# Performance work log

Measured on AMD Instinct MI355X. Metric: run time of the kernel, lower is better.

Reference implementation:

```python
import jax, jax.numpy as jnp
import numpy as np

B, L, H, NH, NB = 8, 200, 128, 4, 2
HD = H // NH
ITEM_NUM, TIME_SPAN = 50000, 256
PAD = -2.0**32 + 1.0


def setup_inputs() -> dict:
    key = jax.random.key(0)
    ks = jax.random.split(key, 32)
    def g(i, shape, s=0.02):
        return jax.random.normal(ks[i], shape, jnp.float32) * s
    item_emb = g(0, (ITEM_NUM + 1, H)).at[0].set(0.0)  # padding_idx=0
    return dict(
        user_ids=jax.random.randint(ks[1], (B,), 0, 1000),
        log_seqs=jax.random.randint(ks[2], (B, L), 0, ITEM_NUM),
        time_matrices=jax.random.randint(ks[3], (B, L, L), 0, TIME_SPAN + 1),
        pos_seqs=jax.random.randint(ks[4], (B, L), 0, ITEM_NUM + 1),
        neg_seqs=jax.random.randint(ks[5], (B, L), 0, ITEM_NUM + 1),
        item_emb=item_emb,
        pos_K_emb=g(6, (L, H)), pos_V_emb=g(7, (L, H)),
        time_K_emb=g(8, (TIME_SPAN + 1, H)), time_V_emb=g(9, (TIME_SPAN + 1, H)),
        attn_ln_g=jnp.ones((NB, H)), attn_ln_b=jnp.zeros((NB, H)),
        Wq=g(10, (NB, H, H)), bq=jnp.zeros((NB, H)),
        Wk=g(11, (NB, H, H)), bk=jnp.zeros((NB, H)),
        Wv=g(12, (NB, H, H)), bv=jnp.zeros((NB, H)),
        fwd_ln_g=jnp.ones((NB, H)), fwd_ln_b=jnp.zeros((NB, H)),
        W1=g(13, (NB, H, H)), b1=jnp.zeros((NB, H)),
        W2=g(14, (NB, H, H)), b2=jnp.zeros((NB, H)),
        last_ln_g=jnp.ones((H,)), last_ln_b=jnp.zeros((H,)),
    )


def _ln(x, g, b, eps=1e-8):
    m = x.mean(-1, keepdims=True)
    v = jnp.var(x, axis=-1, keepdims=True)
    return (x - m) / jnp.sqrt(v + eps) * g + b


def _heads(x):
    # [..., H] -> [NH, ..., HD]; matches torch.cat(torch.split(x, HD, -1), 0)
    y = x.reshape(x.shape[:-1] + (NH, HD))
    return jnp.moveaxis(y, -2, 0)


def reference(user_ids, log_seqs, time_matrices, pos_seqs, neg_seqs, item_emb,
              pos_K_emb, pos_V_emb, time_K_emb, time_V_emb,
              attn_ln_g, attn_ln_b, Wq, bq, Wk, bk, Wv, bv,
              fwd_ln_g, fwd_ln_b, W1, b1, W2, b2, last_ln_g, last_ln_b):
    # user_ids is unused in the original forward as well.
    tmask = log_seqs == 0                                  # [B,L] True = pad
    keep = (~tmask)[..., None].astype(jnp.float32)
    seqs = item_emb[log_seqs] * np.float32(np.sqrt(H))
    seqs = seqs * keep
    pKh = _heads(pos_K_emb)                                # [NH,L,HD]
    pVh = _heads(pos_V_emb)
    tKh = _heads(time_K_emb[time_matrices])                # [NH,B,L,L,HD]
    tVh = _heads(time_V_emb[time_matrices])
    causal = ~jnp.tril(jnp.ones((L, L), bool))             # True above diag -> masked
    bad = tmask[:, :, None] | causal[None]                 # [B,L,L]
    scale = np.float32(np.sqrt(HD))
    for i in range(NB):
        Qin = _ln(seqs, attn_ln_g[i], attn_ln_b[i])
        Qh = _heads(Qin @ Wq[i].T + bq[i])                 # [NH,B,L,HD]
        Kh = _heads(seqs @ Wk[i].T + bk[i])
        Vh = _heads(seqs @ Wv[i].T + bv[i])
        attn = (jnp.einsum('nbqd,nbkd->nbqk', Qh, Kh)
                + jnp.einsum('nbqd,nkd->nbqk', Qh, pKh)
                + jnp.einsum('nbqkd,nbqd->nbqk', tKh, Qh)) / scale
        attn = jnp.where(bad[None], PAD, attn)
        attn = jax.nn.softmax(attn, axis=-1)
        out = (jnp.einsum('nbqk,nbkd->nbqd', attn, Vh)
               + jnp.einsum('nbqk,nkd->nbqd', attn, pVh)
               + jnp.einsum('nbqk,nbqkd->nbqd', attn, tVh))
        out = jnp.moveaxis(out, 0, -2).reshape(seqs.shape)  # merge heads -> [B,L,H]
        seqs = Qin + out                                    # residual uses LN'd Q (as in source)
        seqs = _ln(seqs, fwd_ln_g[i], fwd_ln_b[i])
        ff = jax.nn.relu(seqs @ W1[i].T + b1[i]) @ W2[i].T + b2[i] + seqs
        seqs = ff * keep
    log_feats = _ln(seqs, last_ln_g, last_ln_b)
    pos_logits = (log_feats * item_emb[pos_seqs]).sum(-1)   # [B,L]
    neg_logits = (log_feats * item_emb[neg_seqs]).sum(-1)
    return pos_logits, neg_logits
```

## Files before the change

kernel.cpp:

```cpp
#include <hip/hip_runtime.h>
#include <hip/hip_bf16.h>

#define BB 8
#define LL 200
#define HH 128
#define NHEAD 4
#define HDIM 32
#define NBLK 2
#define BL (BB * LL)
#define NT 257
#define QT 8
#define NQT 25
#define SSP 208
#define KTP 66

static constexpr float SQRT_H    = 11.313708498984761f;
static constexpr float INV_SCALE = 0.17677669529663687f;
static constexpr float PADV      = -4294967295.0f;

__global__ void k_lnqkv(const float* __restrict__ seqs_in,
                        const int* __restrict__ log_seqs,
                        const float* __restrict__ item_emb,
                        const float* __restrict__ g, const float* __restrict__ bia,
                        const float* __restrict__ Wq, const float* __restrict__ bq,
                        const float* __restrict__ Wk, const float* __restrict__ bk,
                        const float* __restrict__ Wv, const float* __restrict__ bv,
                        const float* __restrict__ posK, const float* __restrict__ posV,
                        float* __restrict__ Qin, float* __restrict__ Q,
                        float* __restrict__ K, float* __restrict__ V) {
    int row0 = blockIdx.x * 4;
    int tid = threadIdx.x;
    int wv = tid >> 6, ln = tid & 63;
    __shared__ float xT[HH][8];
    __shared__ float Wst[3 * HH * 33];

    for (int rr = 0; rr < 2; rr++) {
        int r = 2 * wv + rr;
        int row = row0 + r;
        float v0, v1;
        if (seqs_in) {
            v0 = seqs_in[(size_t)row * HH + ln];
            v1 = seqs_in[(size_t)row * HH + ln + 64];
        } else {
            int idx = log_seqs[row];
            if (idx == 0) { v0 = 0.f; v1 = 0.f; }
            else {
                v0 = item_emb[(size_t)idx * HH + ln] * SQRT_H;
                v1 = item_emb[(size_t)idx * HH + ln + 64] * SQRT_H;
            }
        }
        float s = v0 + v1, s2 = v0 * v0 + v1 * v1;
        for (int off = 32; off; off >>= 1) {
            s  += __shfl_xor(s, off);
            s2 += __shfl_xor(s2, off);
        }
        float mean = s * (1.f / HH);
        float var  = s2 * (1.f / HH) - mean * mean;
        float inv  = 1.f / sqrtf(var + 1e-8f);
        float q0v = (v0 - mean) * inv * g[ln]      + bia[ln];
        float q1v = (v1 - mean) * inv * g[ln + 64] + bia[ln + 64];
        xT[ln][r] = q0v;      xT[ln + 64][r] = q1v;
        xT[ln][4 + r] = v0;   xT[ln + 64][4 + r] = v1;
        Qin[(size_t)row * HH + ln]      = q0v;
        Qin[(size_t)row * HH + ln + 64] = q1v;
    }
    __syncthreads();

    int j = tid;
    float aq[4] = {0,0,0,0}, ak[4] = {0,0,0,0}, av[4] = {0,0,0,0};
    for (int c = 0; c < 4; c++) {
        #pragma unroll
        for (int m = 0; m < 3; m++) {
            const float* Wm = (m == 0) ? Wq : (m == 1) ? Wk : Wv;
            #pragma unroll
            for (int p = 0; p < 8; p++) {
                int idx = tid + p * 128;
                int jj = idx >> 3, k4 = idx & 7;
                float4 w = *(const float4*)(Wm + (size_t)jj * HH + c * 32 + k4 * 4);
                float* dst = &Wst[m * HH * 33 + jj * 33 + k4 * 4];
                dst[0] = w.x; dst[1] = w.y; dst[2] = w.z; dst[3] = w.w;
            }
        }
        __syncthreads();
        #pragma unroll 4
        for (int kk = 0; kk < 32; kk++) {
            int k = c * 32 + kk;
            float4 xq4 = *(const float4*)&xT[k][0];
            float4 xs4 = *(const float4*)&xT[k][4];
            float wq = Wst[0 * HH * 33 + j * 33 + kk];
            float wk = Wst[1 * HH * 33 + j * 33 + kk];
            float wvv = Wst[2 * HH * 33 + j * 33 + kk];
            aq[0] += xq4.x * wq; aq[1] += xq4.y * wq; aq[2] += xq4.z * wq; aq[3] += xq4.w * wq;
            ak[0] += xs4.x * wk; ak[1] += xs4.y * wk; ak[2] += xs4.z * wk; ak[3] += xs4.w * wk;
            av[0] += xs4.x * wvv; av[1] += xs4.y * wvv; av[2] += xs4.z * wvv; av[3] += xs4.w * wvv;
        }
        __syncthreads();
    }
    float bqv = bq[j], bkv = bk[j], bvv = bv[j];
    #pragma unroll
    for (int r = 0; r < 4; r++) {
        int row = row0 + r;
        int l = row % LL;
        Q[(size_t)row * HH + j] = (aq[r] + bqv) * INV_SCALE;
        K[(size_t)row * HH + j] = ak[r] + bkv + posK[l * HH + j];
        V[(size_t)row * HH + j] = av[r] + bvv + posV[l * HH + j];
    }
}

__global__ void k_attn(const float* __restrict__ Q, const float* __restrict__ K,
                       const float* __restrict__ V,
                       const float* __restrict__ timeK, const float* __restrict__ timeV,
                       const int* __restrict__ tm,
                       float* __restrict__ att) {
    int bn = blockIdx.x & 31;
    int b = bn >> 2, n = bn & 3;
    int qt = (NQT - 1) - (blockIdx.x >> 5);
    int q0 = qt * QT;
    int kmax = q0 + QT - 1;
    int tid = threadIdx.x;
    int wv = tid >> 6, ln = tid & 63;

    __shared__ float Qs[QT * HDIM];
    __shared__ float KstT[HDIM * KTP];
    __shared__ float DTW[QT * NT];
    __shared__ float Ssc[QT * SSP];
    __shared__ int   tmst[QT * LL];
    __shared__ float Ost[QT * HDIM];

    Ost[tid] = 0.f;
    if (tid < 64) {
        int qi = tid >> 3, d4 = tid & 7;
        *(float4*)(Qs + qi * HDIM + d4 * 4) =
            *(const float4*)(Q + ((size_t)(b * LL + q0 + qi)) * HH + n * HDIM + d4 * 4);
    }
    #pragma unroll
    for (int qi = 0; qi < QT; qi++)
        if (tid < LL)
            tmst[qi * LL + tid] = tm[((size_t)(b * LL + q0 + qi)) * LL + tid];
    __syncthreads();

    int k2 = tid & 31, qi_c = tid >> 5;

    for (int c = 0; c < 5; c++) {
        #pragma unroll
        for (int p = 0; p < 2; p++) {
            int idx = tid + p * 256;
            int r = idx >> 3, d4 = idx & 7;
            int tau = c * 64 + r;
            float4 w = make_float4(0.f, 0.f, 0.f, 0.f);
            if (tau < NT) w = *(const float4*)(timeK + (size_t)tau * HH + n * HDIM + d4 * 4);
            KstT[(d4 * 4 + 0) * KTP + r] = w.x;
            KstT[(d4 * 4 + 1) * KTP + r] = w.y;
            KstT[(d4 * 4 + 2) * KTP + r] = w.z;
            KstT[(d4 * 4 + 3) * KTP + r] = w.w;
        }
        __syncthreads();
        float a0 = 0.f, a1 = 0.f;
        #pragma unroll 4
        for (int d = 0; d < HDIM; d++) {
            float qv = Qs[qi_c * HDIM + d];
            float2 kv = *(const float2*)&KstT[d * KTP + k2 * 2];
            a0 += qv * kv.x; a1 += qv * kv.y;
        }
        int tau0 = c * 64 + k2 * 2;
        if (tau0 < NT)     DTW[qi_c * NT + tau0]     = a0;
        if (tau0 + 1 < NT) DTW[qi_c * NT + tau0 + 1] = a1;
        __syncthreads();
    }

    int nch = (kmax >> 6) + 1;
    for (int c = 0; c < nch; c++) {
        #pragma unroll
        for (int p = 0; p < 2; p++) {
            int idx = tid + p * 256;
            int r = idx >> 3, d4 = idx & 7;
            int k = c * 64 + r;
            float4 w = make_float4(0.f, 0.f, 0.f, 0.f);
            if (k < LL) w = *(const float4*)(K + ((size_t)(b * LL + k)) * HH + n * HDIM + d4 * 4);
            KstT[(d4 * 4 + 0) * KTP + r] = w.x;
            KstT[(d4 * 4 + 1) * KTP + r] = w.y;
            KstT[(d4 * 4 + 2) * KTP + r] = w.z;
            KstT[(d4 * 4 + 3) * KTP + r] = w.w;
        }
        __syncthreads();
        float a0 = 0.f, a1 = 0.f;
        #pragma unroll 4
        for (int d = 0; d < HDIM; d++) {
            float qv = Qs[qi_c * HDIM + d];
            float2 kv = *(const float2*)&KstT[d * KTP + k2 * 2];
            a0 += qv * kv.x; a1 += qv * kv.y;
        }
        int q = q0 + qi_c;
        int k0 = c * 64 + k2 * 2;
        if (k0 <= kmax)
            Ssc[qi_c * SSP + k0] = (k0 <= q) ? (a0 + DTW[qi_c * NT + tmst[qi_c * LL + k0]]) : PADV;
        if (k0 + 1 <= kmax)
            Ssc[qi_c * SSP + k0 + 1] = (k0 + 1 <= q) ? (a1 + DTW[qi_c * NT + tmst[qi_c * LL + k0 + 1]]) : PADV;
        __syncthreads();
    }

    for (int idx = tid; idx < QT * NT; idx += 256) DTW[idx] = 0.f;
    __syncthreads();

    for (int rr = 0; rr < 2; rr++) {
        int qi = wv + rr * 4;
        int q = q0 + qi;
        float sv[4];
        float m = PADV;
        #pragma unroll
        for (int jj = 0; jj < 4; jj++) {
            int k = ln + 64 * jj;
            sv[jj] = (k <= q) ? Ssc[qi * SSP + k] : PADV;
            m = fmaxf(m, sv[jj]);
        }
        for (int off = 32; off; off >>= 1) m = fmaxf(m, __shfl_xor(m, off));
        float sum = 0.f;
        #pragma unroll
        for (int jj = 0; jj < 4; jj++) {
            int k = ln + 64 * jj;
            sv[jj] = (k <= q) ? __expf(sv[jj] - m) : 0.f;
            sum += sv[jj];
        }
        for (int off = 32; off; off >>= 1) sum += __shfl_xor(sum, off);
        float inv = 1.f / sum;
        #pragma unroll
        for (int jj = 0; jj < 4; jj++) {
            int k = ln + 64 * jj;
            float p = sv[jj] * inv;
            if (k < SSP) Ssc[qi * SSP + k] = (k <= q) ? p : 0.f;
            if (k <= q) atomicAdd(&DTW[qi * NT + tmst[qi * LL + k]], p);
        }
    }
    __syncthreads();

    int d = tid & 31, kg = tid >> 5;
    float acc[QT] = {0,0,0,0,0,0,0,0};
    const float* vb = V + ((size_t)(b * LL)) * HH + n * HDIM + d;
    for (int k = kg; k <= kmax; k += 8) {
        float v = vb[(size_t)k * HH];
        #pragma unroll
        for (int qi = 0; qi < QT; qi++) acc[qi] += Ssc[qi * SSP + k] * v;
    }
    const float* tvb = timeV + n * HDIM + d;
    for (int t = kg; t < NT; t += 8) {
        float v = tvb[(size_t)t * HH];
        #pragma unroll
        for (int qi = 0; qi < QT; qi++) acc[qi] += DTW[qi * NT + t] * v;
    }
    #pragma unroll
    for (int qi = 0; qi < QT; qi++) atomicAdd(&Ost[qi * HDIM + d], acc[qi]);
    __syncthreads();
    {
        int qi = tid >> 5;
        att[((size_t)(b * LL + q0 + qi)) * HH + n * HDIM + d] = Ost[qi * HDIM + d];
    }
}

__global__ void k_lnffn(const float* __restrict__ Qin, const float* __restrict__ att,
                        const float* __restrict__ g, const float* __restrict__ bia,
                        const float* __restrict__ W1, const float* __restrict__ b1,
                        const float* __restrict__ W2, const float* __restrict__ b2,
                        const int* __restrict__ log_seqs, float* __restrict__ out) {
    int row0 = blockIdx.x * 4;
    int tid = threadIdx.x;
    int wv = tid >> 6, ln = tid & 63;
    __shared__ float xT[HH][8];
    __shared__ float Wst[HH * 33];

    for (int rr = 0; rr < 2; rr++) {
        int r = 2 * wv + rr;
        int row = row0 + r;
        float v0 = Qin[(size_t)row * HH + ln]      + att[(size_t)row * HH + ln];
        float v1 = Qin[(size_t)row * HH + ln + 64] + att[(size_t)row * HH + ln + 64];
        float s = v0 + v1, s2 = v0 * v0 + v1 * v1;
        for (int off = 32; off; off >>= 1) {
            s  += __shfl_xor(s, off);
            s2 += __shfl_xor(s2, off);
        }
        float mean = s * (1.f / HH);
        float var  = s2 * (1.f / HH) - mean * mean;
        float inv  = 1.f / sqrtf(var + 1e-8f);
        xT[ln][r]      = (v0 - mean) * inv * g[ln]      + bia[ln];
        xT[ln + 64][r] = (v1 - mean) * inv * g[ln + 64] + bia[ln + 64];
    }
    __syncthreads();

    int j = tid;
    float a[4] = {0,0,0,0};
    for (int c = 0; c < 4; c++) {
        #pragma unroll
        for (int p = 0; p < 8; p++) {
            int idx = tid + p * 128;
            int jj = idx >> 3, k4 = idx & 7;
            float4 w = *(const float4*)(W1 + (size_t)jj * HH + c * 32 + k4 * 4);
            float* dst = &Wst[jj * 33 + k4 * 4];
            dst[0] = w.x; dst[1] = w.y; dst[2] = w.z; dst[3] = w.w;
        }
        __syncthreads();
        #pragma unroll 4
        for (int kk = 0; kk < 32; kk++) {
            int k = c * 32 + kk;
            float4 x4 = *(const float4*)&xT[k][0];
            float w = Wst[j * 33 + kk];
            a[0] += x4.x * w; a[1] += x4.y * w; a[2] += x4.z * w; a[3] += x4.w * w;
        }
        __syncthreads();
    }
    float b1v = b1[j];
    #pragma unroll
    for (int r = 0; r < 4; r++) {
        float t = a[r] + b1v;
        xT[j][4 + r] = t > 0.f ? t : 0.f;
    }
    __syncthreads();

    float c2[4] = {0,0,0,0};
    for (int c = 0; c < 4; c++) {
        #pragma unroll
        for (int p = 0; p < 8; p++) {
            int idx = tid + p * 128;
            int jj = idx >> 3, k4 = idx & 7;
            float4 w = *(const float4*)(W2 + (size_t)jj * HH + c * 32 + k4 * 4);
            float* dst = &Wst[jj * 33 + k4 * 4];
            dst[0] = w.x; dst[1] = w.y; dst[2] = w.z; dst[3] = w.w;
        }
        __syncthreads();
        #pragma unroll 4
        for (int kk = 0; kk < 32; kk++) {
            int k = c * 32 + kk;
            float4 x4 = *(const float4*)&xT[k][4];
            float w = Wst[j * 33 + kk];
            c2[0] += x4.x * w; c2[1] += x4.y * w; c2[2] += x4.z * w; c2[3] += x4.w * w;
        }
        __syncthreads();
    }
    float b2v = b2[j];
    float4 y4 = *(const float4*)&xT[j][0];
    float yv[4] = {y4.x, y4.y, y4.z, y4.w};
    #pragma unroll
    for (int r = 0; r < 4; r++) {
        int row = row0 + r;
        float t = c2[r] + b2v + yv[r];
        out[(size_t)row * HH + j] = (log_seqs[row] == 0) ? 0.f : t;
    }
}

__global__ void k_lnlogits(const float* __restrict__ seqs,
                           const float* __restrict__ g, const float* __restrict__ bia,
                           const float* __restrict__ item_emb,
                           const int* __restrict__ pos, const int* __restrict__ neg,
                           float* __restrict__ out) {
    int row = blockIdx.x;
    int h = threadIdx.x;
    float v = seqs[(size_t)row * HH + h];
    float s = v, s2 = v * v;
    for (int off = 32; off; off >>= 1) {
        s  += __shfl_xor(s, off);
        s2 += __shfl_xor(s2, off);
    }
    __shared__ float r1[2], r2[2];
    if ((h & 63) == 0) { r1[h >> 6] = s; r2[h >> 6] = s2; }
    __syncthreads();
    float mean = (r1[0] + r1[1]) * (1.f / HH);
    float var  = (r2[0] + r2[1]) * (1.f / HH) - mean * mean;
    float inv = 1.f / sqrtf(var + 1e-8f);
    float f = (v - mean) * inv * g[h] + bia[h];

    int ip = pos[row], in_ = neg[row];
    float vp = f * item_emb[(size_t)ip * HH + h];
    float vn = f * item_emb[(size_t)in_ * HH + h];
    for (int off = 32; off; off >>= 1) {
        vp += __shfl_xor(vp, off);
        vn += __shfl_xor(vn, off);
    }
    __shared__ float rp[2], rn[2];
    if ((h & 63) == 0) { rp[h >> 6] = vp; rn[h >> 6] = vn; }
    __syncthreads();
    if (h == 0) {
        out[row]      = rp[0] + rp[1];
        out[BL + row] = rn[0] + rn[1];
    }
}

extern "C" void kernel_launch(void* const* d_in, const int* in_sizes, int n_in,
                              void* d_out, int out_size, void* d_ws, size_t ws_size,
                              hipStream_t stream) {
    const int* log_seqs   = (const int*)d_in[1];
    const int* tm         = (const int*)d_in[2];
    const int* pos_seqs   = (const int*)d_in[3];
    const int* neg_seqs   = (const int*)d_in[4];
    const float* item_emb = (const float*)d_in[5];
    const float* posK     = (const float*)d_in[6];
    const float* posV     = (const float*)d_in[7];
    const float* timeK    = (const float*)d_in[8];
    const float* timeV    = (const float*)d_in[9];
    const float* attn_g   = (const float*)d_in[10];
    const float* attn_b   = (const float*)d_in[11];
    const float* Wq       = (const float*)d_in[12];
    const float* bq       = (const float*)d_in[13];
    const float* Wk       = (const float*)d_in[14];
    const float* bk       = (const float*)d_in[15];
    const float* Wv       = (const float*)d_in[16];
    const float* bv       = (const float*)d_in[17];
    const float* fwd_g    = (const float*)d_in[18];
    const float* fwd_b    = (const float*)d_in[19];
    const float* W1       = (const float*)d_in[20];
    const float* b1       = (const float*)d_in[21];
    const float* W2       = (const float*)d_in[22];
    const float* b2       = (const float*)d_in[23];
    const float* last_g   = (const float*)d_in[24];
    const float* last_b   = (const float*)d_in[25];

    float* seqs = (float*)d_ws;
    float* Qin  = seqs + (size_t)BL * HH;
    float* Qb   = Qin  + (size_t)BL * HH;
    float* Kb   = Qb   + (size_t)BL * HH;
    float* Vb   = Kb   + (size_t)BL * HH;
    float* att  = Vb   + (size_t)BL * HH;

    for (int i = 0; i < NBLK; i++) {
        k_lnqkv<<<BL / 4, 128, 0, stream>>>(i == 0 ? nullptr : seqs, log_seqs, item_emb,
                                            attn_g + i * HH, attn_b + i * HH,
                                            Wq + (size_t)i * HH * HH, bq + i * HH,
                                            Wk + (size_t)i * HH * HH, bk + i * HH,
                                            Wv + (size_t)i * HH * HH, bv + i * HH,
                                            posK, posV, Qin, Qb, Kb, Vb);
        k_attn<<<NQT * 32, 256, 0, stream>>>(Qb, Kb, Vb, timeK, timeV, tm, att);
        k_lnffn<<<BL / 4, 128, 0, stream>>>(Qin, att, fwd_g + i * HH, fwd_b + i * HH,
                                            W1 + (size_t)i * HH * HH, b1 + i * HH,
                                            W2 + (size_t)i * HH * HH, b2 + i * HH,
                                            log_seqs, seqs);
    }
    k_lnlogits<<<BL, HH, 0, stream>>>(seqs, last_g, last_b, item_emb,
                                      pos_seqs, neg_seqs, (float*)d_out);
}
```

Baseline: 269.9 us.

## Retile QKV and FFN projections as register-blocked GEMMs with larger row tiles

Replaces the 4-row-per-block QKV and fused FFN kernels with tiled GEMM kernels: QKV uses 32-row by 64-column tiles split across the three matrices, and the FFN is split into two kernels (ff1 with LN+W1+ReLU, ff2 with W2 plus residual recomputed from Qin+att). Each thread computes a small register tile from shared memory, and the full 128-wide K dimension is loaded at once. The aim is to cut how often weights are reloaded per row and to raise arithmetic intensity. In exchange it adds an extra launch, an h1 intermediate buffer round trip, and LayerNorm recomputed redundantly across column tiles.

```diff
diff --git a/kernel.cpp b/kernel.cpp
--- a/kernel.cpp
+++ b/kernel.cpp
@@ -13,97 +13,153 @@
 #define NQT 25
 #define SSP 208
 #define KTP 66
+#define ASP 36
+#define BSP 66
+#define FASP 20
+#define RSP 132
 
 static constexpr float SQRT_H    = 11.313708498984761f;
 static constexpr float INV_SCALE = 0.17677669529663687f;
 static constexpr float PADV      = -4294967295.0f;
 
-__global__ void k_lnqkv(const float* __restrict__ seqs_in,
-                        const int* __restrict__ log_seqs,
-                        const float* __restrict__ item_emb,
-                        const float* __restrict__ g, const float* __restrict__ bia,
-                        const float* __restrict__ Wq, const float* __restrict__ bq,
-                        const float* __restrict__ Wk, const float* __restrict__ bk,
-                        const float* __restrict__ Wv, const float* __restrict__ bv,
-                        const float* __restrict__ posK, const float* __restrict__ posV,
-                        float* __restrict__ Qin, float* __restrict__ Q,
-                        float* __restrict__ K, float* __restrict__ V) {
-    int row0 = blockIdx.x * 4;
+__global__ void k_qkv_gemm(const float* __restrict__ seqs_in,
+                           const int* __restrict__ log_seqs,
+                           const float* __restrict__ item_emb,
+                           const float* __restrict__ g, const float* __restrict__ bia,
+                           const float* __restrict__ Wq, const float* __restrict__ bq,
+                           const float* __restrict__ Wk, const float* __restrict__ bk,
+                           const float* __restrict__ Wv, const float* __restrict__ bv,
+                           const float* __restrict__ posK, const float* __restrict__ posV,
+                           float* __restrict__ Qin, float* __restrict__ Q,
+                           float* __restrict__ K, float* __restrict__ V) {
+    int mt = blockIdx.x / 6, nt = blockIdx.x % 6;
+    int matsel = nt >> 1;
+    int jb = (nt & 1) * 64;
+    int row0 = mt * 32;
     int tid = threadIdx.x;
-    int wv = tid >> 6, ln = tid & 63;
-    __shared__ float xT[HH][8];
-    __shared__ float Wst[3 * HH * 33];
-
-    for (int rr = 0; rr < 2; rr++) {
-        int r = 2 * wv + rr;
+    __shared__ float As[128 * ASP];
+    __shared__ float Bs[128 * BSP];
+
+    {
+        int r = tid >> 3, seg = tid & 7;
         int row = row0 + r;
-        float v0, v1;
+        float4 vv[4];
         if (seqs_in) {
-            v0 = seqs_in[(size_t)row * HH + ln];
-            v1 = seqs_in[(size_t)row * HH + ln + 64];
+            #pragma unroll
+            for (int i = 0; i < 4; i++)
+                vv[i] = *(const float4*)(seqs_in + (size_t)row * HH + seg * 16 + i * 4);
         } else {
             int idx = log_seqs[row];
-            if (idx == 0) { v0 = 0.f; v1 = 0.f; }
-            else {
-                v0 = item_emb[(size_t)idx * HH + ln] * SQRT_H;
-                v1 = item_emb[(size_t)idx * HH + ln + 64] * SQRT_H;
+            if (idx == 0) {
+                #pragma unroll
+                for (int i = 0; i < 4; i++) vv[i] = make_float4(0.f, 0.f, 0.f, 0.f);
+            } else {
+                #pragma unroll
+                for (int i = 0; i < 4; i++) {
+                    float4 e = *(const float4*)(item_emb + (size_t)idx * HH + seg * 16 + i * 4);
+                    vv[i] = make_float4(e.x * SQRT_H, e.y * SQRT_H, e.z * SQRT_H, e.w * SQRT_H);
+                }
             }
         }
-        float s = v0 + v1, s2 = v0 * v0 + v1 * v1;
-        for (int off = 32; off; off >>= 1) {
-            s  += __shfl_xor(s, off);
-            s2 += __shfl_xor(s2, off);
-        }
-        float mean = s * (1.f / HH);
-        float var  = s2 * (1.f / HH) - mean * mean;
-        float inv  = 1.f / sqrtf(var + 1e-8f);
-        float q0v = (v0 - mean) * inv * g[ln]      + bia[ln];
-        float q1v = (v1 - mean) * inv * g[ln + 64] + bia[ln + 64];
-        xT[ln][r] = q0v;      xT[ln + 64][r] = q1v;
-        xT[ln][4 + r] = v0;   xT[ln + 64][4 + r] = v1;
-        Qin[(size_t)row * HH + ln]      = q0v;
-        Qin[(size_t)row * HH + ln + 64] = q1v;
-    }
-    __syncthreads();
-
-    int j = tid;
-    float aq[4] = {0,0,0,0}, ak[4] = {0,0,0,0}, av[4] = {0,0,0,0};
-    for (int c = 0; c < 4; c++) {
-        #pragma unroll
-        for (int m = 0; m < 3; m++) {
-            const float* Wm = (m == 0) ? Wq : (m == 1) ? Wk : Wv;
+        if (matsel == 0) {
+            float s = 0.f, s2 = 0.f;
             #pragma unroll
-            for (int p = 0; p < 8; p++) {
-                int idx = tid + p * 128;
-                int jj = idx >> 3, k4 = idx & 7;
-                float4 w = *(const float4*)(Wm + (size_t)jj * HH + c * 32 + k4 * 4);
-                float* dst = &Wst[m * HH * 33 + jj * 33 + k4 * 4];
-                dst[0] = w.x; dst[1] = w.y; dst[2] = w.z; dst[3] = w.w;
+            for (int i = 0; i < 4; i++) {
+                s  += vv[i].x + vv[i].y + vv[i].z + vv[i].w;
+                s2 += vv[i].x * vv[i].x + vv[i].y * vv[i].y + vv[i].z * vv[i].z + vv[i].w * vv[i].w;
             }
-        }
-        __syncthreads();
-        #pragma unroll 4
-        for (int kk = 0; kk < 32; kk++) {
-            int k = c * 32 + kk;
-            float4 xq4 = *(const float4*)&xT[k][0];
-            float4 xs4 = *(const float4*)&xT[k][4];
-            float wq = Wst[0 * HH * 33 + j * 33 + kk];
-            float wk = Wst[1 * HH * 33 + j * 33 + kk];
-            float wvv = Wst[2 * HH * 33 + j * 33 + kk];
-            aq[0] += xq4.x * wq; aq[1] += xq4.y * wq; aq[2] += xq4.z * wq; aq[3] += xq4.w * wq;
-            ak[0] += xs4.x * wk; ak[1] += xs4.y * wk; ak[2] += xs4.z * wk; ak[3] += xs4.w * wk;
-            av[0] += xs4.x * wvv; av[1] += xs4.y * wvv; av[2] += xs4.z * wvv; av[3] += xs4.w * wvv;
-        }
-        __syncthreads();
-    }
-    float bqv = bq[j], bkv = bk[j], bvv = bv[j];
-    #pragma unroll
-    for (int r = 0; r < 4; r++) {
-        int row = row0 + r;
-        int l = row % LL;
-        Q[(size_t)row * HH + j] = (aq[r] + bqv) * INV_SCALE;
-        K[(size_t)row * HH + j] = ak[r] + bkv + posK[l * HH + j];
-        V[(size_t)row * HH + j] = av[r] + bvv + posV[l * HH + j];
+            #pragma unroll
+            for (int off = 1; off < 8; off <<= 1) {
+                s  += __shfl_xor(s, off);
+                s2 += __shfl_xor(s2, off);
+            }
+            float mean = s * (1.f / HH);
+            float var  = s2 * (1.f / HH) - mean * mean;
+            float inv  = 1.f / sqrtf(var + 1e-8f);
+            #pragma unroll
+            for (int i = 0; i < 4; i++) {
+                int k = seg * 16 + i * 4;
+                float4 g4 = *(const float4*)(g + k);
+                float4 b4 = *(const float4*)(bia + k);
+                float4 y;
+                y.x = (vv[i].x - mean) * inv * g4.x + b4.x;
+                y.y = (vv[i].y - mean) * inv * g4.y + b4.y;
+                y.z = (vv[i].z - mean) * inv * g4.z + b4.z;
+                y.w = (vv[i].w - mean) * inv * g4.w + b4.w;
+                As[(k + 0) * ASP + r] = y.x;
+                As[(k + 1) * ASP + r] = y.y;
+                As[(k + 2) * ASP + r] = y.z;
+                As[(k + 3) * ASP + r] = y.w;
+                if (nt == 0) *(float4*)(Qin + (size_t)row * HH + k) = y;
+            }
+        } else {
+            #pragma unroll
+            for (int i = 0; i < 4; i++) {
+                int k = seg * 16 + i * 4;
+                As[(k + 0) * ASP + r] = vv[i].x;
+                As[(k + 1) * ASP + r] = vv[i].y;
+                As[(k + 2) * ASP + r] = vv[i].z;
+                As[(k + 3) * ASP + r] = vv[i].w;
+            }
+        }
+    }
+    {
+        const float* W = (matsel == 0) ? Wq : (matsel == 1) ? Wk : Wv;
+        int k4 = tid & 31, jj0 = tid >> 5;
+        #pragma unroll
+        for (int p = 0; p < 8; p++) {
+            int jj = jj0 + p * 8;
+            float4 w = *(const float4*)(W + (size_t)(jb + jj) * HH + k4 * 4);
+            Bs[(k4 * 4 + 0) * BSP + jj] = w.x;
+            Bs[(k4 * 4 + 1) * BSP + jj] = w.y;
+            Bs[(k4 * 4 + 2) * BSP + jj] = w.z;
+            Bs[(k4 * 4 + 3) * BSP + jj] = w.w;
+        }
+    }
+    __syncthreads();
+
+    int my = tid >> 5, jx = tid & 31;
+    float a00=0,a01=0,a10=0,a11=0,a20=0,a21=0,a30=0,a31=0;
+    #pragma unroll 4
+    for (int k = 0; k < HH; k++) {
+        float4 a = *(const float4*)&As[k * ASP + my * 4];
+        float2 b = *(const float2*)&Bs[k * BSP + jx * 2];
+        a00 += a.x * b.x; a01 += a.x * b.y;
+        a10 += a.y * b.x; a11 += a.y * b.y;
+        a20 += a.z * b.x; a21 += a.z * b.y;
+        a30 += a.w * b.x; a31 += a.w * b.y;
+    }
+    float accs[4][2] = {{a00,a01},{a10,a11},{a20,a21},{a30,a31}};
+    int col = jb + jx * 2;
+    if (matsel == 0) {
+        float2 bb = *(const float2*)(bq + col);
+        #pragma unroll
+        for (int r = 0; r < 4; r++) {
+            int row = row0 + my * 4 + r;
+            float2 o = make_float2((accs[r][0] + bb.x) * INV_SCALE,
+                                   (accs[r][1] + bb.y) * INV_SCALE);
+            *(float2*)(Q + (size_t)row * HH + col) = o;
+        }
+    } else if (matsel == 1) {
+        float2 bb = *(const float2*)(bk + col);
+        #pragma unroll
+        for (int r = 0; r < 4; r++) {
+            int row = row0 + my * 4 + r;
+            int l = row % LL;
+            float2 pk = *(const float2*)(posK + (size_t)l * HH + col);
+            float2 o = make_float2(accs[r][0] + bb.x + pk.x, accs[r][1] + bb.y + pk.y);
+            *(float2*)(K + (size_t)row * HH + col) = o;
+        }
+    } else {
+        float2 bb = *(const float2*)(bv + col);
+        #pragma unroll
+        for (int r = 0; r < 4; r++) {
+            int row = row0 + my * 4 + r;
+            int l = row % LL;
+            float2 pv = *(const float2*)(posV + (size_t)l * HH + col);
+            float2 o = make_float2(accs[r][0] + bb.x + pv.x, accs[r][1] + bb.y + pv.y);
+            *(float2*)(V + (size_t)row * HH + col) = o;
+        }
     }
 }
 
@@ -256,92 +312,173 @@
     }
 }
 
-__global__ void k_lnffn(const float* __restrict__ Qin, const float* __restrict__ att,
-                        const float* __restrict__ g, const float* __restrict__ bia,
-                        const float* __restrict__ W1, const float* __restrict__ b1,
-                        const float* __restrict__ W2, const float* __restrict__ b2,
-                        const int* __restrict__ log_seqs, float* __restrict__ out) {
-    int row0 = blockIdx.x * 4;
+__global__ void k_ff1(const float* __restrict__ Qin, const float* __restrict__ att,
+                      const float* __restrict__ g, const float* __restrict__ bia,
+                      const float* __restrict__ W1, const float* __restrict__ b1,
+                      float* __restrict__ h1) {
+    int mt = blockIdx.x >> 1, nt = blockIdx.x & 1;
+    int jb = nt * 64;
+    int row0 = mt * 16;
     int tid = threadIdx.x;
-    int wv = tid >> 6, ln = tid & 63;
-    __shared__ float xT[HH][8];
-    __shared__ float Wst[HH * 33];
-
-    for (int rr = 0; rr < 2; rr++) {
-        int r = 2 * wv + rr;
+    __shared__ float As[128 * FASP];
+    __shared__ float Bs[128 * BSP];
+
+    {
+        int r = tid >> 4, seg = tid & 15;
         int row = row0 + r;
-        float v0 = Qin[(size_t)row * HH + ln]      + att[(size_t)row * HH + ln];
-        float v1 = Qin[(size_t)row * HH + ln + 64] + att[(size_t)row * HH + ln + 64];
-        float s = v0 + v1, s2 = v0 * v0 + v1 * v1;
-        for (int off = 32; off; off >>= 1) {
+        float4 vv[2];
+        #pragma unroll
+        for (int i = 0; i < 2; i++) {
+            int k = seg * 8 + i * 4;
+            float4 q4 = *(const float4*)(Qin + (size_t)row * HH + k);
+            float4 a4 = *(const float4*)(att + (size_t)row * HH + k);
+            vv[i] = make_float4(q4.x + a4.x, q4.y + a4.y, q4.z + a4.z, q4.w + a4.w);
+        }
+        float s = 0.f, s2 = 0.f;
+        #pragma unroll
+        for (int i = 0; i < 2; i++) {
+            s  += vv[i].x + vv[i].y + vv[i].z + vv[i].w;
+            s2 += vv[i].x * vv[i].x + vv[i].y * vv[i].y + vv[i].z * vv[i].z + vv[i].w * vv[i].w;
+        }
+        #pragma unroll
+        for (int off = 1; off < 16; off <<= 1) {
             s  += __shfl_xor(s, off);
             s2 += __shfl_xor(s2, off);
         }
         float mean = s * (1.f / HH);
         float var  = s2 * (1.f / HH) - mean * mean;
         float inv  = 1.f / sqrtf(var + 1e-8f);
-        xT[ln][r]      = (v0 - mean) * inv * g[ln]      + bia[ln];
-        xT[ln + 64][r] = (v1 - mean) * inv * g[ln + 64] + bia[ln + 64];
-    }
-    __syncthreads();
-
-    int j = tid;
-    float a[4] = {0,0,0,0};
-    for (int c = 0; c < 4; c++) {
+        #pragma unroll
+        for (int i = 0; i < 2; i++) {
+            int k = seg * 8 + i * 4;
+            float4 g4 = *(const float4*)(g + k);
+            float4 b4 = *(const float4*)(bia + k);
+            As[(k + 0) * FASP + r] = (vv[i].x - mean) * inv * g4.x + b4.x;
+            As[(k + 1) * FASP + r] = (vv[i].y - mean) * inv * g4.y + b4.y;
+            As[(k + 2) * FASP + r] = (vv[i].z - mean) * inv * g4.z + b4.z;
+            As[(k + 3) * FASP + r] = (vv[i].w - mean) * inv * g4.w + b4.w;
+        }
+    }
+    {
+        int k4 = tid & 31, jj0 = tid >> 5;
         #pragma unroll
         for (int p = 0; p < 8; p++) {
-            int idx = tid + p * 128;
-            int jj = idx >> 3, k4 = idx & 7;
-            float4 w = *(const float4*)(W1 + (size_t)jj * HH + c * 32 + k4 * 4);
-            float* dst = &Wst[jj * 33 + k4 * 4];
-            dst[0] = w.x; dst[1] = w.y; dst[2] = w.z; dst[3] = w.w;
-        }
-        __syncthreads();
-        #pragma unroll 4
-        for (int kk = 0; kk < 32; kk++) {
-            int k = c * 32 + kk;
-            float4 x4 = *(const float4*)&xT[k][0];
-            float w = Wst[j * 33 + kk];
-            a[0] += x4.x * w; a[1] += x4.y * w; a[2] += x4.z * w; a[3] += x4.w * w;
-        }
-        __syncthreads();
-    }
-    float b1v = b1[j];
+            int jj = jj0 + p * 8;
+            float4 w = *(const float4*)(W1 + (size_t)(jb + jj) * HH + k4 * 4);
+            Bs[(k4 * 4 + 0) * BSP + jj] = w.x;
+            Bs[(k4 * 4 + 1) * BSP + jj] = w.y;
+            Bs[(k4 * 4 + 2) * BSP + jj] = w.z;
+            Bs[(k4 * 4 + 3) * BSP + jj] = w.w;
+        }
+    }
+    __syncthreads();
+
+    int my = tid >> 5, jx = tid & 31;
+    float a00 = 0, a01 = 0, a10 = 0, a11 = 0;
+    #pragma unroll 4
+    for (int k = 0; k < HH; k++) {
+        float2 a = *(const float2*)&As[k * FASP + my * 2];
+        float2 b = *(const float2*)&Bs[k * BSP + jx * 2];
+        a00 += a.x * b.x; a01 += a.x * b.y;
+        a10 += a.y * b.x; a11 += a.y * b.y;
+    }
+    int col = jb + jx * 2;
+    float2 bb = *(const float2*)(b1 + col);
+    {
+        int row = row0 + my * 2;
+        float2 o0 = make_float2(fmaxf(a00 + bb.x, 0.f), fmaxf(a01 + bb.y, 0.f));
+        float2 o1 = make_float2(fmaxf(a10 + bb.x, 0.f), fmaxf(a11 + bb.y, 0.f));
+        *(float2*)(h1 + (size_t)row * HH + col) = o0;
+        *(float2*)(h1 + (size_t)(row + 1) * HH + col) = o1;
+    }
+}
+
+__global__ void k_ff2(const float* __restrict__ h1,
+                      const float* __restrict__ Qin, const float* __restrict__ att,
+                      const float* __restrict__ g, const float* __restrict__ bia,
+                      const float* __restrict__ W2, const float* __restrict__ b2,
+                      const int* __restrict__ log_seqs,
+                      float* __restrict__ out) {
+    int mt = blockIdx.x >> 1, nt = blockIdx.x & 1;
+    int jb = nt * 64;
+    int row0 = mt * 16;
+    int tid = threadIdx.x;
+    __shared__ float As[128 * FASP];
+    __shared__ float Bs[128 * BSP];
+    __shared__ float Rs[16 * RSP];
+    __shared__ float mu[16], rstd[16];
+
+    {
+        int r = tid >> 4, seg = tid & 15;
+        int row = row0 + r;
+        #pragma unroll
+        for (int i = 0; i < 2; i++) {
+            int k = seg * 8 + i * 4;
+            float4 h4 = *(const float4*)(h1 + (size_t)row * HH + k);
+            As[(k + 0) * FASP + r] = h4.x;
+            As[(k + 1) * FASP + r] = h4.y;
+            As[(k + 2) * FASP + r] = h4.z;
+            As[(k + 3) * FASP + r] = h4.w;
+        }
+        float s = 0.f, s2 = 0.f;
+        #pragma unroll
+        for (int i = 0; i < 2; i++) {
+            int k = seg * 8 + i * 4;
+            float4 q4 = *(const float4*)(Qin + (size_t)row * HH + k);
+            float4 a4 = *(const float4*)(att + (size_t)row * HH + k);
+            float4 v = make_float4(q4.x + a4.x, q4.y + a4.y, q4.z + a4.z, q4.w + a4.w);
+            *(float4*)(Rs + r * RSP + k) = v;
+            s  += v.x + v.y + v.z + v.w;
+            s2 += v.x * v.x + v.y * v.y + v.z * v.z + v.w * v.w;
+        }
+        #pragma unroll
+        for (int off = 1; off < 16; off <<= 1) {
+            s  += __shfl_xor(s, off);
+            s2 += __shfl_xor(s2, off);
+        }
+        float mean = s * (1.f / HH);
+        float var  = s2 * (1.f / HH) - mean * mean;
+        if (seg == 0) { mu[r] = mean; rstd[r] = 1.f / sqrtf(var + 1e-8f); }
+    }
+    {
+        int k4 = tid & 31, jj0 = tid >> 5;
+        #pragma unroll
+        for (int p = 0; p < 8; p++) {
+            int jj = jj0 + p * 8;
+            float4 w = *(const float4*)(W2 + (size_t)(jb + jj) * HH + k4 * 4);
+            Bs[(k4 * 4 + 0) * BSP + jj] = w.x;
+            Bs[(k4 * 4 + 1) * BSP + jj] = w.y;
+            Bs[(k4 * 4 + 2) * BSP + jj] = w.z;
+            Bs[(k4 * 4 + 3) * BSP + jj] = w.w;
+        }
+    }
+    __syncthreads();
+
+    int my = tid >> 5, jx = tid & 31;
+    float a00 = 0, a01 = 0, a10 = 0, a11 = 0;
+    #pragma unroll 4
+    for (int k = 0; k < HH; k++) {
+        float2 a = *(const float2*)&As[k * FASP + my * 2];
+        float2 b = *(const float2*)&Bs[k * BSP + jx * 2];
+        a00 += a.x * b.x; a01 += a.x * b.y;
+        a10 += a.y * b.x; a11 += a.y * b.y;
+    }
+    int col = jb + jx * 2;
+    float2 bb = *(const float2*)(b2 + col);
+    float2 g2 = *(const float2*)(g + col);
+    float2 lb = *(const float2*)(bia + col);
+    float accs[2][2] = {{a00, a01}, {a10, a11}};
     #pragma unroll
-    for (int r = 0; r < 4; r++) {
-        float t = a[r] + b1v;
-        xT[j][4 + r] = t > 0.f ? t : 0.f;
-    }
-    __syncthreads();
-
-    float c2[4] = {0,0,0,0};
-    for (int c = 0; c < 4; c++) {
-        #pragma unroll
-        for (int p = 0; p < 8; p++) {
-            int idx = tid + p * 128;
-            int jj = idx >> 3, k4 = idx & 7;
-            float4 w = *(const float4*)(W2 + (size_t)jj * HH + c * 32 + k4 * 4);
-            float* dst = &Wst[jj * 33 + k4 * 4];
-            dst[0] = w.x; dst[1] = w.y; dst[2] = w.z; dst[3] = w.w;
-        }
-        __syncthreads();
-        #pragma unroll 4
-        for (int kk = 0; kk < 32; kk++) {
-            int k = c * 32 + kk;
-            float4 x4 = *(const float4*)&xT[k][4];
-            float w = Wst[j * 33 + kk];
-            c2[0] += x4.x * w; c2[1] += x4.y * w; c2[2] += x4.z * w; c2[3] += x4.w * w;
-        }
-        __syncthreads();
-    }
-    float b2v = b2[j];
-    float4 y4 = *(const float4*)&xT[j][0];
-    float yv[4] = {y4.x, y4.y, y4.z, y4.w};
-    #pragma unroll
-    for (int r = 0; r < 4; r++) {
-        int row = row0 + r;
-        float t = c2[r] + b2v + yv[r];
-        out[(size_t)row * HH + j] = (log_seqs[row] == 0) ? 0.f : t;
+    for (int r = 0; r < 2; r++) {
+        int ri = my * 2 + r;
+        int row = row0 + ri;
+        float m = mu[ri], iv = rstd[ri];
+        float2 R = *(const float2*)&Rs[ri * RSP + col];
+        float y0 = (R.x - m) * iv * g2.x + lb.x;
+        float y1 = (R.y - m) * iv * g2.y + lb.y;
+        float2 o = make_float2(accs[r][0] + bb.x + y0, accs[r][1] + bb.y + y1);
+        if (log_seqs[row] == 0) o = make_float2(0.f, 0.f);
+        *(float2*)(out + (size_t)row * HH + col) = o;
     }
 }
 
@@ -417,19 +554,21 @@
     float* Kb   = Qb   + (size_t)BL * HH;
     float* Vb   = Kb   + (size_t)BL * HH;
     float* att  = Vb   + (size_t)BL * HH;
+    float* h1   = att  + (size_t)BL * HH;
 
     for (int i = 0; i < NBLK; i++) {
-        k_lnqkv<<<BL / 4, 128, 0, stream>>>(i == 0 ? nullptr : seqs, log_seqs, item_emb,
+        k_qkv_gemm<<<300, 256, 0, stream>>>(i == 0 ? nullptr : seqs, log_seqs, item_emb,
                                             attn_g + i * HH, attn_b + i * HH,
                                             Wq + (size_t)i * HH * HH, bq + i * HH,
                                             Wk + (size_t)i * HH * HH, bk + i * HH,
                                             Wv + (size_t)i * HH * HH, bv + i * HH,
                                             posK, posV, Qin, Qb, Kb, Vb);
         k_attn<<<NQT * 32, 256, 0, stream>>>(Qb, Kb, Vb, timeK, timeV, tm, att);
-        k_lnffn<<<BL / 4, 128, 0, stream>>>(Qin, att, fwd_g + i * HH, fwd_b + i * HH,
-                                            W1 + (size_t)i * HH * HH, b1 + i * HH,
-                                            W2 + (size_t)i * HH * HH, b2 + i * HH,
-                                            log_seqs, seqs);
+        k_ff1<<<200, 256, 0, stream>>>(Qin, att, fwd_g + i * HH, fwd_b + i * HH,
+                                       W1 + (size_t)i * HH * HH, b1 + i * HH, h1);
+        k_ff2<<<200, 256, 0, stream>>>(h1, Qin, att, fwd_g + i * HH, fwd_b + i * HH,
+                                       W2 + (size_t)i * HH * HH, b2 + i * HH,
+                                       log_seqs, seqs);
     }
     k_lnlogits<<<BL, HH, 0, stream>>>(seqs, last_g, last_b, item_emb,
                                       pos_seqs, neg_seqs, (float*)d_out);
```

Result: faster. 241.0 us (-10.7%).
